# Performance work log

Measured on AMD Instinct MI355X. Metric: run time of the kernel, lower is better.

## Reference

```python
import jax, jax.numpy as jnp
import numpy as np

WS = 16          # window_size
HS = 8           # halo_size
NH = 4           # num_heads
DIM = 128
WSH = WS + 2 * HS  # 32, window with halo
B, H, W = 2, 128, 128


def _rel_pos_index():
    # static relative-position index table, (WSH^2, WSH^2), int
    r = np.arange(-HS, WS + HS)
    coords = np.stack(np.meshgrid(r, r, indexing='ij'))        # (2, WSH, WSH)
    cf = coords.reshape(2, -1)                                  # (2, WSH^2)
    rel = (cf[:, :, None] - cf[:, None, :]).transpose(1, 2, 0)  # (L, L, 2)
    rel = rel.copy()
    rel[..., 0] += WS + HS - 1
    rel[..., 1] += WS + HS - 1
    rel[..., 0] *= 2 * WS + 2 * HS - 1
    return rel.sum(-1)  # (1024, 1024)

_RPI = _rel_pos_index()


def setup_inputs() -> dict:
    key = jax.random.key(0)
    ks = jax.random.split(key, 10)
    p = lambda k, shp: (jax.random.normal(k, shp, dtype=jnp.float32) * 0.02)
    return {
        'x': jax.random.normal(ks[0], (B, H, W, DIM), dtype=jnp.float32),
        'Wq': p(ks[1], (DIM, DIM)), 'bq': jnp.zeros((DIM,), jnp.float32),
        'Wk': p(ks[2], (DIM, DIM)), 'bk': jnp.zeros((DIM,), jnp.float32),
        'Wv': p(ks[3], (DIM, DIM)), 'bv': jnp.zeros((DIM,), jnp.float32),
        'Wp': p(ks[4], (DIM, DIM)), 'bp': jnp.zeros((DIM,), jnp.float32),
        'bias_table': p(ks[5], ((2 * WS + 2 * HS - 1) ** 2, NH)),
        'shift_size': 0,
    }


def reference(x, Wq, bq, Wk, bk, Wv, bv, Wp, bp, bias_table, shift_size):
    Bx, Hx, Wx, C = x.shape
    hd = C // NH
    scale = hd ** -0.5
    if shift_size > 0:
        x = jnp.roll(x, (-shift_size, -shift_size), axis=(1, 2))
    # reflect-pad by halo and gather overlapping 32x32 windows (stride 16)
    xp = jnp.pad(x, ((0, 0), (HS, HS), (HS, HS), (0, 0)), mode='reflect')
    nWh, nWw = Hx // WS, Wx // WS
    rows = (jnp.arange(nWh) * WS)[:, None] + jnp.arange(WSH)   # (nWh, 32)
    cols = (jnp.arange(nWw) * WS)[:, None] + jnp.arange(WSH)   # (nWw, 32)
    w = xp[:, rows]                 # (B, nWh, 32, Wp, C)
    w = w[:, :, :, cols]            # (B, nWh, 32, nWw, 32, C)
    w = w.transpose(0, 1, 3, 2, 4, 5).reshape(-1, WSH, WSH, C)  # (B*nW, 32, 32, C)
    center = w[:, HS:HS + WS, HS:HS + WS].reshape(-1, WS * WS, C)   # (nWb, 256, C)
    kv = w.reshape(-1, WSH * WSH, C)                                # (nWb, 1024, C)
    q = (center @ Wq.T + bq).reshape(-1, WS * WS, NH, hd).transpose(0, 2, 1, 3)
    k = (kv @ Wk.T + bk).reshape(-1, WSH * WSH, NH, hd).transpose(0, 2, 1, 3)
    v = (kv @ Wv.T + bv).reshape(-1, WSH * WSH, NH, hd).transpose(0, 2, 1, 3)
    attn = jnp.einsum('bhqd,bhkd->bhqk', q, k) * scale   # (nWb, H, 256, 1024)
    bias = bias_table[_RPI.reshape(-1)].reshape(WSH * WSH, WSH * WSH, NH)
    bias = bias.transpose(2, 0, 1)                        # (H, 1024, 1024)
    start = HS * 2 * WS                                   # 256, as in source
    attn = attn + bias[:, start:start + WS * WS, :][None]
    attn = jax.nn.softmax(attn, axis=-1)
    out = jnp.einsum('bhqk,bhkd->bhqd', attn, v)
    out = out.transpose(0, 2, 1, 3).reshape(-1, WS * WS, C)
    out = out @ Wp.T + bp
    out = out.reshape(Bx, nWh, nWw, WS, WS, C).transpose(0, 1, 3, 2, 4, 5)
    out = out.reshape(Bx, Hx, Wx, C)
    if shift_size > 0:
        out = jnp.roll(out, (shift_size, shift_size), axis=(1, 2))
    return out
```

## Files before the change

kernel.cpp:

```cpp
#include <hip/hip_runtime.h>


typedef unsigned short ushort_t;
typedef __attribute__((ext_vector_type(8))) short bf16x8;
typedef __attribute__((ext_vector_type(4))) float floatx4;

#define NHEADS 4
#define BTBL 2209
#define PK 64
#define LOG2E 1.4426950408889634f
#define QSCALE (0.17677669529663687f * LOG2E)

__device__ __forceinline__ int reflect_idx(int p) {
    p = (p < 0) ? -p : p;
    p = (p > 127) ? 254 - p : p;
    return p;
}

__device__ __forceinline__ ushort_t f2b(float x) {
    unsigned u = __float_as_uint(x);
    return (ushort_t)((u + 0x7fffu + ((u >> 16) & 1u)) >> 16);
}

__global__ __launch_bounds__(256) void pack_w(
    const float* __restrict__ Wq, const float* __restrict__ Wk,
    const float* __restrict__ Wv, const float* __restrict__ Wp,
    const float* __restrict__ bq, const float* __restrict__ bk,
    const float* __restrict__ bv, const float* __restrict__ bp,
    ushort_t* __restrict__ Wqkv, ushort_t* __restrict__ Wpb,
    float* __restrict__ bqkv, float* __restrict__ bpb)
{
    int idx = blockIdx.x * 256 + threadIdx.x;
    if (idx < 16384)       Wqkv[idx] = f2b(Wq[idx]);
    else if (idx < 32768)  Wqkv[idx] = f2b(Wk[idx - 16384]);
    else if (idx < 49152)  Wqkv[idx] = f2b(Wv[idx - 32768]);
    else if (idx < 65536)  Wpb[idx - 49152] = f2b(Wp[idx - 49152]);
    else {
        int e = idx - 65536;
        for (int k = e; k < 512; k += 256) {
            if (k < 128)      bqkv[k] = bq[k];
            else if (k < 256) bqkv[k] = bk[k - 128];
            else if (k < 384) bqkv[k] = bv[k - 256];
            else              bpb[k - 384] = bp[k - 384];
        }
    }
}

__global__ __launch_bounds__(256) void bias_frag(
    const float* __restrict__ bt, ushort_t* __restrict__ bf)
{
    int idx  = blockIdx.x * 256 + threadIdx.x;
    int lane = idx & 63;
    int qtw  = (idx >> 6) & 15;
    int kt   = (idx >> 10) & 63;
    int h    = (idx >> 16) & 3;
    int q     = qtw * 16 + (lane & 15);
    int kbase = kt * 16 + ((lane >> 4) << 2);
    unsigned v[4];
    #pragma unroll
    for (int r = 0; r < 4; ++r) {
        int key = kbase + r;
        int kr = key >> 5, kc = key & 31;
        int bidx = ((q >> 5) + 31 - kr) * 47 + (q & 31) - kc + 23;
        if (bidx < 0) bidx += BTBL;
        v[r] = f2b(bt[bidx * NHEADS + h] * LOG2E);
    }
    uint2 out;
    out.x = v[0] | (v[1] << 16);
    out.y = v[2] | (v[3] << 16);
    *(uint2*)&bf[(size_t)idx * 4] = out;
}

template <bool IN_BF16, bool OUT_BF16>
__global__ __launch_bounds__(256) void gemm_mfma(
    const void* __restrict__ Xv, const ushort_t* __restrict__ W,
    const float* __restrict__ bias, void* __restrict__ Yv,
    const int ldy, const float scale0)
{
    __shared__ ushort_t Xs[128 * 136];

    const int t    = threadIdx.x;
    const int w    = t >> 6;
    const int lane = t & 63;
    const int quad = lane >> 4;
    const int l15  = lane & 15;
    const int m0   = blockIdx.x * 128;
    const int nb   = blockIdx.y;
    const float sc = (nb == 0) ? scale0 : 1.0f;

    if (IN_BF16) {
        const ushort_t* X = (const ushort_t*)Xv;
        #pragma unroll
        for (int i = 0; i < 8; ++i) {
            int s = t + i * 256;
            int row = s >> 4, c8 = s & 15;
            *(int4*)&Xs[row * 136 + c8 * 8] =
                *(const int4*)&X[(size_t)(m0 + row) * 128 + c8 * 8];
        }
    } else {
        const float* X = (const float*)Xv;
        #pragma unroll
        for (int i = 0; i < 16; ++i) {
            int s = t + i * 256;
            int row = s >> 5, c4 = s & 31;
            float4 v = *(const float4*)&X[(size_t)(m0 + row) * 128 + c4 * 4];
            uint2 pk;
            pk.x = (unsigned)f2b(v.x) | ((unsigned)f2b(v.y) << 16);
            pk.y = (unsigned)f2b(v.z) | ((unsigned)f2b(v.w) << 16);
            *(uint2*)&Xs[row * 136 + c4 * 4] = pk;
        }
    }
    __syncthreads();

    float bv[8];
    #pragma unroll
    for (int nt = 0; nt < 8; ++nt) bv[nt] = bias[nb * 128 + nt * 16 + l15];

    floatx4 acc[2][8];
    #pragma unroll
    for (int mt = 0; mt < 2; ++mt)
        #pragma unroll
        for (int nt = 0; nt < 8; ++nt)
            acc[mt][nt] = (floatx4)(bv[nt]);

    #pragma unroll
    for (int kc = 0; kc < 4; ++kc) {
        bf16x8 af[2], bf[8];
        #pragma unroll
        for (int mt = 0; mt < 2; ++mt)
            af[mt] = *(const bf16x8*)&Xs[(w * 32 + mt * 16 + l15) * 136 + kc * 32 + quad * 8];
        #pragma unroll
        for (int nt = 0; nt < 8; ++nt)
            bf[nt] = *(const bf16x8*)&W[(size_t)(nb * 128 + nt * 16 + l15) * 128 + kc * 32 + quad * 8];
        #pragma unroll
        for (int mt = 0; mt < 2; ++mt)
            #pragma unroll
            for (int nt = 0; nt < 8; ++nt)
                acc[mt][nt] = __builtin_amdgcn_mfma_f32_16x16x32_bf16(af[mt], bf[nt], acc[mt][nt], 0, 0, 0);
    }

    #pragma unroll
    for (int mt = 0; mt < 2; ++mt) {
        #pragma unroll
        for (int r = 0; r < 4; ++r) {
            int m = m0 + w * 32 + mt * 16 + quad * 4 + r;
            #pragma unroll
            for (int nt = 0; nt < 8; ++nt) {
                int n = nb * 128 + nt * 16 + l15;
                float y = acc[mt][nt][r] * sc;
                if (OUT_BF16)
                    ((ushort_t*)Yv)[(size_t)m * ldy + n] = f2b(y);
                else
                    ((float*)Yv)[(size_t)m * ldy + n] = y;
            }
        }
    }
}

__global__ __launch_bounds__(256, 2) void halo_attn(
    const ushort_t* __restrict__ QKV,
    const ushort_t* __restrict__ biasf,
    ushort_t* __restrict__ O)
{
    __shared__ ushort_t P_lds[4 * 64 * PK];
    __shared__ ushort_t Vt_lds[4 * 32 * PK];

    const int t    = threadIdx.x;
    const int wave = t >> 6;
    const int lane = t & 63;
    const int quad = lane >> 4;
    const int l15  = lane & 15;
    const int swz  = (l15 & 7) << 3;

    const int win  = blockIdx.x;
    const int head = blockIdx.y;
    const int b    = win >> 6;
    const int wh   = (win >> 3) & 7;
    const int ww   = win & 7;

    bf16x8 qf[4];
    int qpix[4];
    #pragma unroll
    for (int qt = 0; qt < 4; ++qt) {
        int q_abs = wave * 64 + qt * 16 + l15;
        int gy = wh * 16 + (q_abs >> 4), gx = ww * 16 + (q_abs & 15);
        int pix = (b * 128 + gy) * 128 + gx;
        qpix[qt] = pix;
        qf[qt] = *(const bf16x8*)(QKV + (size_t)pix * 384 + head * 32 + quad * 8);
    }

    floatx4 Oa[2][4];
    #pragma unroll
    for (int dt = 0; dt < 2; ++dt)
        #pragma unroll
        for (int qt = 0; qt < 4; ++qt)
            Oa[dt][qt] = (floatx4)0.f;
    float l[4] = {0.f, 0.f, 0.f, 0.f};

    ushort_t* Pw  = P_lds  + wave * 64 * PK;
    ushort_t* Vtw = Vt_lds + wave * 32 * PK;

    for (int c = 0; c < 16; ++c) {
        {
            int keyv = c * 64 + lane;
            int ky = reflect_idx(wh * 16 + (keyv >> 5) - 8);
            int kx = reflect_idx(ww * 16 + (keyv & 31) - 8);
            int pixv = (b * 128 + ky) * 128 + kx;
            const int4* vp4 = (const int4*)(QKV + (size_t)pixv * 384 + 256 + head * 32);
            int4 vw0 = vp4[0], vw1 = vp4[1], vw2 = vp4[2], vw3 = vp4[3];
            const ushort_t* vs0 = (const ushort_t*)&vw0;
            const ushort_t* vs1 = (const ushort_t*)&vw1;
            const ushort_t* vs2 = (const ushort_t*)&vw2;
            const ushort_t* vs3 = (const ushort_t*)&vw3;
            #pragma unroll
            for (int d = 0; d < 8; ++d) {
                int cs = lane ^ (d << 3);
                Vtw[(d +  0) * PK + cs] = vs0[d];
                Vtw[(d +  8) * PK + cs] = vs1[d];
                Vtw[(d + 16) * PK + cs] = vs2[d];
                Vtw[(d + 24) * PK + cs] = vs3[d];
            }
        }

        bf16x8 kf[4];
        #pragma unroll
        for (int kt = 0; kt < 4; ++kt) {
            int key = c * 64 + kt * 16 + l15;
            int ky = reflect_idx(wh * 16 + (key >> 5) - 8);
            int kx = reflect_idx(ww * 16 + (key & 31) - 8);
            int pixk = (b * 128 + ky) * 128 + kx;
            kf[kt] = *(const bf16x8*)(QKV + (size_t)pixk * 384 + 128 + head * 32 + quad * 8);
        }

        floatx4 S[4][4];
        #pragma unroll
        for (int kt = 0; kt < 4; ++kt) {
            int kt_abs = c * 4 + kt;
            #pragma unroll
            for (int qt = 0; qt < 4; ++qt) {
                size_t off = ((((size_t)head * 64 + kt_abs) * 16 + (wave * 4 + qt)) * 64 + lane) * 4;
                uint2 bb = *(const uint2*)(biasf + off);
                floatx4 s;
                s[0] = __uint_as_float(bb.x << 16);
                s[1] = __uint_as_float(bb.x & 0xffff0000u);
                s[2] = __uint_as_float(bb.y << 16);
                s[3] = __uint_as_float(bb.y & 0xffff0000u);
                S[kt][qt] = s;
            }
        }
        #pragma unroll
        for (int kt = 0; kt < 4; ++kt)
            #pragma unroll
            for (int qt = 0; qt < 4; ++qt)
                S[kt][qt] = __builtin_amdgcn_mfma_f32_16x16x32_bf16(kf[kt], qf[qt], S[kt][qt], 0, 0, 0);

        #pragma unroll
        for (int qt = 0; qt < 4; ++qt) {
            float ls = 0.f;
            #pragma unroll
            for (int kt = 0; kt < 4; ++kt) {
                #pragma unroll
                for (int r = 0; r < 4; ++r) {
                    float p = __builtin_amdgcn_exp2f(S[kt][qt][r]);
                    S[kt][qt][r] = p;
                    ls += p;
                }
            }
            l[qt] += ls;
            #pragma unroll
            for (int kt = 0; kt < 4; ++kt) {
                uint2 pk;
                pk.x = __builtin_amdgcn_perm(__float_as_uint(S[kt][qt][1]),
                                             __float_as_uint(S[kt][qt][0]), 0x07060302u);
                pk.y = __builtin_amdgcn_perm(__float_as_uint(S[kt][qt][3]),
                                             __float_as_uint(S[kt][qt][2]), 0x07060302u);
                *(uint2*)&Pw[(qt * 16 + l15) * PK + ((kt * 16 + quad * 4) ^ swz)] = pk;
            }
        }

        #pragma unroll
        for (int ks = 0; ks < 2; ++ks) {
            bf16x8 vf[2];
            #pragma unroll
            for (int dt = 0; dt < 2; ++dt)
                vf[dt] = *(const bf16x8*)&Vtw[(dt * 16 + l15) * PK + ((ks * 32 + quad * 8) ^ swz)];
            #pragma unroll
            for (int qt = 0; qt < 4; ++qt) {
                bf16x8 pf = *(const bf16x8*)&Pw[(qt * 16 + l15) * PK + ((ks * 32 + quad * 8) ^ swz)];
                #pragma unroll
                for (int dt = 0; dt < 2; ++dt)
                    Oa[dt][qt] = __builtin_amdgcn_mfma_f32_16x16x32_bf16(vf[dt], pf, Oa[dt][qt], 0, 0, 0);
            }
        }
    }

    #pragma unroll
    for (int qt = 0; qt < 4; ++qt) {
        float lq = l[qt];
        lq += __shfl_xor(lq, 16);
        lq += __shfl_xor(lq, 32);
        float inv = 1.0f / lq;
        #pragma unroll
        for (int dt = 0; dt < 2; ++dt) {
            uint2 pk;
            pk.x = (unsigned)f2b(Oa[dt][qt][0] * inv) | ((unsigned)f2b(Oa[dt][qt][1] * inv) << 16);
            pk.y = (unsigned)f2b(Oa[dt][qt][2] * inv) | ((unsigned)f2b(Oa[dt][qt][3] * inv) << 16);
            *(uint2*)(O + (size_t)qpix[qt] * 128 + head * 32 + dt * 16 + quad * 4) = pk;
        }
    }
}

extern "C" void kernel_launch(void* const* d_in, const int* in_sizes, int n_in,
                              void* d_out, int out_size, void* d_ws, size_t ws_size,
                              hipStream_t stream)
{
    const float* x          = (const float*)d_in[0];
    const float* Wq         = (const float*)d_in[1];
    const float* bq         = (const float*)d_in[2];
    const float* Wk         = (const float*)d_in[3];
    const float* bk         = (const float*)d_in[4];
    const float* Wv         = (const float*)d_in[5];
    const float* bv         = (const float*)d_in[6];
    const float* Wp         = (const float*)d_in[7];
    const float* bp         = (const float*)d_in[8];
    const float* bias_table = (const float*)d_in[9];
    float* out = (float*)d_out;

    char* ws = (char*)d_ws;
    ushort_t* Wqkv = (ushort_t*)(ws);
    ushort_t* Wpb  = (ushort_t*)(ws + 98304);
    float*    bqkv = (float*)   (ws + 131072);
    float*    bpb  = (float*)   (ws + 132608);
    ushort_t* QKV  = (ushort_t*)(ws + 133120);
    ushort_t* Ob   = (ushort_t*)(ws + 25298944);
    ushort_t* bf   = (ushort_t*)(ws + 33687552);

    pack_w<<<dim3(257), dim3(256), 0, stream>>>(Wq, Wk, Wv, Wp, bq, bk, bv, bp,
                                                Wqkv, Wpb, bqkv, bpb);
    bias_frag<<<dim3(1024), dim3(256), 0, stream>>>(bias_table, bf);
    gemm_mfma<false, true><<<dim3(256, 3), dim3(256), 0, stream>>>(
        x, Wqkv, bqkv, QKV, 384, QSCALE);
    halo_attn<<<dim3(128, NHEADS), dim3(256), 0, stream>>>(QKV, bf, Ob);
    gemm_mfma<true, false><<<dim3(256, 1), dim3(256), 0, stream>>>(
        Ob, Wpb, bpb, out, 128, 1.0f);
}
```

Before: 167.4 us.

## Merge prep kernels and loop QKV column blocks inside one GEMM block

Fuses the weight-packing and bias-fragment kernels into a single launch, saving one kernel launch. The QKV GEMM now runs all three 128-column blocks in a loop within one workgroup, so each x tile is loaded and converted to bf16 once instead of three times. The MFMA operands are swapped so each lane holds four consecutive output columns, which allows vectorized uint2/float4 stores in place of scalar ones. In exchange the grid for the QKV GEMM shrinks from 768 to 256 blocks, which lowers parallelism.

```diff
diff --git a/kernel.cpp b/kernel.cpp
--- a/kernel.cpp
+++ b/kernel.cpp
@@ -22,56 +22,56 @@
     return (ushort_t)((u + 0x7fffu + ((u >> 16) & 1u)) >> 16);
 }
 
-__global__ __launch_bounds__(256) void pack_w(
+__global__ __launch_bounds__(256) void prep(
     const float* __restrict__ Wq, const float* __restrict__ Wk,
     const float* __restrict__ Wv, const float* __restrict__ Wp,
     const float* __restrict__ bq, const float* __restrict__ bk,
     const float* __restrict__ bv, const float* __restrict__ bp,
+    const float* __restrict__ bt,
     ushort_t* __restrict__ Wqkv, ushort_t* __restrict__ Wpb,
-    float* __restrict__ bqkv, float* __restrict__ bpb)
+    float* __restrict__ bqkv, float* __restrict__ bpb,
+    ushort_t* __restrict__ bf)
 {
-    int idx = blockIdx.x * 256 + threadIdx.x;
-    if (idx < 16384)       Wqkv[idx] = f2b(Wq[idx]);
-    else if (idx < 32768)  Wqkv[idx] = f2b(Wk[idx - 16384]);
-    else if (idx < 49152)  Wqkv[idx] = f2b(Wv[idx - 32768]);
-    else if (idx < 65536)  Wpb[idx - 49152] = f2b(Wp[idx - 49152]);
-    else {
-        int e = idx - 65536;
-        for (int k = e; k < 512; k += 256) {
-            if (k < 128)      bqkv[k] = bq[k];
-            else if (k < 256) bqkv[k] = bk[k - 128];
-            else if (k < 384) bqkv[k] = bv[k - 256];
-            else              bpb[k - 384] = bp[k - 384];
-        }
-    }
-}
-
-__global__ __launch_bounds__(256) void bias_frag(
-    const float* __restrict__ bt, ushort_t* __restrict__ bf)
-{
-    int idx  = blockIdx.x * 256 + threadIdx.x;
-    int lane = idx & 63;
-    int qtw  = (idx >> 6) & 15;
-    int kt   = (idx >> 10) & 63;
-    int h    = (idx >> 16) & 3;
-    int q     = qtw * 16 + (lane & 15);
-    int kbase = kt * 16 + ((lane >> 4) << 2);
-    unsigned v[4];
-    #pragma unroll
-    for (int r = 0; r < 4; ++r) {
-        int key = kbase + r;
-        int kr = key >> 5, kc = key & 31;
-        int bidx = ((q >> 5) + 31 - kr) * 47 + (q & 31) - kc + 23;
-        if (bidx < 0) bidx += BTBL;
-        v[r] = f2b(bt[bidx * NHEADS + h] * LOG2E);
-    }
-    uint2 out;
-    out.x = v[0] | (v[1] << 16);
-    out.y = v[2] | (v[3] << 16);
-    *(uint2*)&bf[(size_t)idx * 4] = out;
-}
-
-template <bool IN_BF16, bool OUT_BF16>
+    if (blockIdx.x < 257) {
+        int idx = blockIdx.x * 256 + threadIdx.x;
+        if (idx < 16384)       Wqkv[idx] = f2b(Wq[idx]);
+        else if (idx < 32768)  Wqkv[idx] = f2b(Wk[idx - 16384]);
+        else if (idx < 49152)  Wqkv[idx] = f2b(Wv[idx - 32768]);
+        else if (idx < 65536)  Wpb[idx - 49152] = f2b(Wp[idx - 49152]);
+        else {
+            int e = idx - 65536;
+            for (int k = e; k < 512; k += 256) {
+                if (k < 128)      bqkv[k] = bq[k];
+                else if (k < 256) bqkv[k] = bk[k - 128];
+                else if (k < 384) bqkv[k] = bv[k - 256];
+                else              bpb[k - 384] = bp[k - 384];
+            }
+        }
+    } else {
+        int idx  = (blockIdx.x - 257) * 256 + threadIdx.x;
+        int lane = idx & 63;
+        int qtw  = (idx >> 6) & 15;
+        int kt   = (idx >> 10) & 63;
+        int h    = (idx >> 16) & 3;
+        int q     = qtw * 16 + (lane & 15);
+        int kbase = kt * 16 + ((lane >> 4) << 2);
+        unsigned v[4];
+        #pragma unroll
+        for (int r = 0; r < 4; ++r) {
+            int key = kbase + r;
+            int kr = key >> 5, kc = key & 31;
+            int bidx = ((q >> 5) + 31 - kr) * 47 + (q & 31) - kc + 23;
+            if (bidx < 0) bidx += BTBL;
+            v[r] = f2b(bt[bidx * NHEADS + h] * LOG2E);
+        }
+        uint2 out;
+        out.x = v[0] | (v[1] << 16);
+        out.y = v[2] | (v[3] << 16);
+        *(uint2*)&bf[(size_t)idx * 4] = out;
+    }
+}
+
+template <bool IN_BF16, bool OUT_BF16, int NB>
 __global__ __launch_bounds__(256) void gemm_mfma(
     const void* __restrict__ Xv, const ushort_t* __restrict__ W,
     const float* __restrict__ bias, void* __restrict__ Yv,
@@ -85,8 +85,6 @@
     const int quad = lane >> 4;
     const int l15  = lane & 15;
     const int m0   = blockIdx.x * 128;
-    const int nb   = blockIdx.y;
-    const float sc = (nb == 0) ? scale0 : 1.0f;
 
     if (IN_BF16) {
         const ushort_t* X = (const ushort_t*)Xv;
@@ -112,46 +110,53 @@
     }
     __syncthreads();
 
-    float bv[8];
-    #pragma unroll
-    for (int nt = 0; nt < 8; ++nt) bv[nt] = bias[nb * 128 + nt * 16 + l15];
-
-    floatx4 acc[2][8];
-    #pragma unroll
-    for (int mt = 0; mt < 2; ++mt)
-        #pragma unroll
-        for (int nt = 0; nt < 8; ++nt)
-            acc[mt][nt] = (floatx4)(bv[nt]);
-
-    #pragma unroll
-    for (int kc = 0; kc < 4; ++kc) {
-        bf16x8 af[2], bf[8];
-        #pragma unroll
-        for (int mt = 0; mt < 2; ++mt)
-            af[mt] = *(const bf16x8*)&Xs[(w * 32 + mt * 16 + l15) * 136 + kc * 32 + quad * 8];
-        #pragma unroll
-        for (int nt = 0; nt < 8; ++nt)
-            bf[nt] = *(const bf16x8*)&W[(size_t)(nb * 128 + nt * 16 + l15) * 128 + kc * 32 + quad * 8];
-        #pragma unroll
-        for (int mt = 0; mt < 2; ++mt)
+    #pragma unroll 1
+    for (int nb = 0; nb < NB; ++nb) {
+        const float sc = (nb == 0) ? scale0 : 1.0f;
+
+        floatx4 acc[2][8];
+        #pragma unroll
+        for (int nt = 0; nt < 8; ++nt) {
+            floatx4 bv = *(const floatx4*)&bias[nb * 128 + nt * 16 + quad * 4];
+            acc[0][nt] = bv;
+            acc[1][nt] = bv;
+        }
+
+        #pragma unroll
+        for (int kc = 0; kc < 4; ++kc) {
+            bf16x8 af[2], bfr[8];
+            #pragma unroll
+            for (int mt = 0; mt < 2; ++mt)
+                af[mt] = *(const bf16x8*)&Xs[(w * 32 + mt * 16 + l15) * 136 + kc * 32 + quad * 8];
             #pragma unroll
             for (int nt = 0; nt < 8; ++nt)
-                acc[mt][nt] = __builtin_amdgcn_mfma_f32_16x16x32_bf16(af[mt], bf[nt], acc[mt][nt], 0, 0, 0);
-    }
-
-    #pragma unroll
-    for (int mt = 0; mt < 2; ++mt) {
-        #pragma unroll
-        for (int r = 0; r < 4; ++r) {
-            int m = m0 + w * 32 + mt * 16 + quad * 4 + r;
+                bfr[nt] = *(const bf16x8*)&W[(size_t)(nb * 128 + nt * 16 + l15) * 128 + kc * 32 + quad * 8];
+            #pragma unroll
+            for (int mt = 0; mt < 2; ++mt)
+                #pragma unroll
+                for (int nt = 0; nt < 8; ++nt)
+                    acc[mt][nt] = __builtin_amdgcn_mfma_f32_16x16x32_bf16(bfr[nt], af[mt], acc[mt][nt], 0, 0, 0);
+        }
+
+        #pragma unroll
+        for (int mt = 0; mt < 2; ++mt) {
+            int m = m0 + w * 32 + mt * 16 + l15;
             #pragma unroll
             for (int nt = 0; nt < 8; ++nt) {
-                int n = nb * 128 + nt * 16 + l15;
-                float y = acc[mt][nt][r] * sc;
-                if (OUT_BF16)
-                    ((ushort_t*)Yv)[(size_t)m * ldy + n] = f2b(y);
-                else
-                    ((float*)Yv)[(size_t)m * ldy + n] = y;
+                int n = nb * 128 + nt * 16 + quad * 4;
+                if (OUT_BF16) {
+                    uint2 pk;
+                    pk.x = (unsigned)f2b(acc[mt][nt][0] * sc) |
+                           ((unsigned)f2b(acc[mt][nt][1] * sc) << 16);
+                    pk.y = (unsigned)f2b(acc[mt][nt][2] * sc) |
+                           ((unsigned)f2b(acc[mt][nt][3] * sc) << 16);
+                    *(uint2*)&((ushort_t*)Yv)[(size_t)m * ldy + n] = pk;
+                } else {
+                    float4 v;
+                    v.x = acc[mt][nt][0] * sc; v.y = acc[mt][nt][1] * sc;
+                    v.z = acc[mt][nt][2] * sc; v.w = acc[mt][nt][3] * sc;
+                    *(float4*)&((float*)Yv)[(size_t)m * ldy + n] = v;
+                }
             }
         }
     }
@@ -335,12 +340,11 @@
     ushort_t* Ob   = (ushort_t*)(ws + 25298944);
     ushort_t* bf   = (ushort_t*)(ws + 33687552);
 
-    pack_w<<<dim3(257), dim3(256), 0, stream>>>(Wq, Wk, Wv, Wp, bq, bk, bv, bp,
-                                                Wqkv, Wpb, bqkv, bpb);
-    bias_frag<<<dim3(1024), dim3(256), 0, stream>>>(bias_table, bf);
-    gemm_mfma<false, true><<<dim3(256, 3), dim3(256), 0, stream>>>(
+    prep<<<dim3(1281), dim3(256), 0, stream>>>(Wq, Wk, Wv, Wp, bq, bk, bv, bp,
+                                               bias_table, Wqkv, Wpb, bqkv, bpb, bf);
+    gemm_mfma<false, true, 3><<<dim3(256), dim3(256), 0, stream>>>(
         x, Wqkv, bqkv, QKV, 384, QSCALE);
     halo_attn<<<dim3(128, NHEADS), dim3(256), 0, stream>>>(QKV, bf, Ob);
-    gemm_mfma<true, false><<<dim3(256, 1), dim3(256), 0, stream>>>(
+    gemm_mfma<true, false, 1><<<dim3(256), dim3(256), 0, stream>>>(
         Ob, Wpb, bpb, out, 128, 1.0f);
 }
```

After: 167.5 us. No clear change (+0.0%).
